# Kernel optimization log

Hardware: AMD Instinct MI355X
Metric: run time of the kernel (lower is better)

Reference implementation:

```python
import jax, jax.numpy as jnp
import numpy as np


def rotary_pos_emb(x):
    # x: [..., seq, dim], dim even. Interleaved (GPT-NeoX-style pairwise) rotary.
    dim, seq = x.shape[-1], x.shape[-2]
    ts = jnp.arange(0, dim, 2, dtype=jnp.float32)
    inv_freqs = 10000.0 ** (-ts / dim)
    grid = jnp.arange(seq, dtype=jnp.float32)[:, None] * inv_freqs[None, :]  # [s, dim//2]
    sin = jnp.repeat(jnp.sin(grid), 2, axis=-1).astype(x.dtype)  # [s, dim]
    cos = jnp.repeat(jnp.cos(grid), 2, axis=-1).astype(x.dtype)  # [s, dim]
    x1, x2 = x[..., ::2], x[..., 1::2]
    xs = jnp.stack([-x2, x1], axis=-1).reshape(x.shape)  # interleave (-x2, x1)
    return x * cos + xs * sin


def setup_inputs() -> dict:
    key = jax.random.key(0)
    kx, kq, kk, kv, ko = jax.random.split(key, 5)
    B, S, D = 2, 2048, 1024
    scale = 1.0 / np.sqrt(D)
    x = jax.random.normal(kx, (B, S, D), dtype=jnp.float32)
    mask = jnp.tril(jnp.ones((S, S), dtype=bool))  # causal
    Wq = jax.random.normal(kq, (D, D), dtype=jnp.float32) * scale
    Wk = jax.random.normal(kk, (D, D), dtype=jnp.float32) * scale
    Wv = jax.random.normal(kv, (D, D), dtype=jnp.float32) * scale
    Wo = jax.random.normal(ko, (D, D), dtype=jnp.float32) * scale
    return {"x": x, "mask": mask, "Wq": Wq, "Wk": Wk, "Wv": Wv, "Wo": Wo}


def reference(x, mask, Wq, Wk, Wv, Wo):
    H = 16
    POS_PORTION = 0.5
    B, S, D = x.shape
    K = D // H
    p = int(K * POS_PORTION)

    q = (x @ Wq) / (K ** 0.5)
    q = q.reshape(B, S, H, K).transpose(0, 2, 1, 3)  # b h l k
    q = jnp.concatenate([rotary_pos_emb(q[..., :p]), q[..., p:]], axis=-1)

    k = (x @ Wk).reshape(B, S, H, K).transpose(0, 2, 1, 3)
    k = jnp.concatenate([rotary_pos_emb(k[..., :p]), k[..., p:]], axis=-1)

    v = (x @ Wv).reshape(B, S, H, K).transpose(0, 2, 1, 3)

    logits = jnp.einsum('bhik,bhjk->bhij', q, k)
    # full-precision masked softmax
    l32 = logits.astype(jnp.float32)
    l32 = jnp.where(mask, l32, -1e30)
    a = jax.nn.softmax(l32, axis=-1).astype(logits.dtype)

    y = jnp.einsum('bhij,bhjv->bhiv', a, v)
    y = y.transpose(0, 2, 1, 3).reshape(B, S, D)  # b l (h v)
    return y @ Wo
```

## Files before the change

### kernel.cpp

```cpp
#include <hip/hip_runtime.h>
#include <cstdint>
#include <cstddef>

typedef __bf16 bf16;
typedef __bf16 bf16x8 __attribute__((ext_vector_type(8)));
typedef float  f32x4  __attribute__((ext_vector_type(4)));

#define B_  2
#define S_  2048
#define D_  1024
#define H_  16
#define KH  64

__device__ __forceinline__ void gload_lds16(const bf16* gp, bf16* lds_base) {
    __builtin_amdgcn_global_load_lds(
        (const __attribute__((address_space(1))) unsigned int*)gp,
        (__attribute__((address_space(3))) unsigned int*)lds_base,
        16, 0, 0);
}

__global__ __launch_bounds__(256) void prep(
    const float* __restrict__ x, bf16* __restrict__ xb,
    const float* __restrict__ Wq, const float* __restrict__ Wk,
    const float* __restrict__ Wv, const float* __restrict__ Wo,
    bf16* __restrict__ WqkvT, bf16* __restrict__ WoT)
{
    __shared__ bf16 tl[64][72];
    int z = blockIdx.x;
    if (z < 4096) {
        const int i = (z * 256 + threadIdx.x) * 4;
        const float4 v = *(const float4*)(x + i);
        union { int2 w; bf16 e[4]; } u;
        u.e[0] = (bf16)v.x; u.e[1] = (bf16)v.y;
        u.e[2] = (bf16)v.z; u.e[3] = (bf16)v.w;
        *(int2*)(xb + i) = u.w;
        return;
    }
    z -= 4096;
    const int zx = z & 15, zy = (z >> 4) & 15, zw = z >> 8;
    const float* src = (zw == 0) ? Wq : (zw == 1) ? Wk : (zw == 2) ? Wv : Wo;
    bf16* dst = (zw < 3) ? (WqkvT + (size_t)zw * D_ * D_) : WoT;
    const int r0 = zy * 64;
    const int c0 = zx * 64;
    const int t  = threadIdx.x;
    {
        const int r = t >> 2, cs = (t & 3) * 16;
        const float4* p = (const float4*)(src + (size_t)(r0 + r) * D_ + c0 + cs);
        float4 a0 = p[0], a1 = p[1], a2 = p[2], a3 = p[3];
        tl[cs +  0][r] = (bf16)a0.x; tl[cs +  1][r] = (bf16)a0.y;
        tl[cs +  2][r] = (bf16)a0.z; tl[cs +  3][r] = (bf16)a0.w;
        tl[cs +  4][r] = (bf16)a1.x; tl[cs +  5][r] = (bf16)a1.y;
        tl[cs +  6][r] = (bf16)a1.z; tl[cs +  7][r] = (bf16)a1.w;
        tl[cs +  8][r] = (bf16)a2.x; tl[cs +  9][r] = (bf16)a2.y;
        tl[cs + 10][r] = (bf16)a2.z; tl[cs + 11][r] = (bf16)a2.w;
        tl[cs + 12][r] = (bf16)a3.x; tl[cs + 13][r] = (bf16)a3.y;
        tl[cs + 14][r] = (bf16)a3.z; tl[cs + 15][r] = (bf16)a3.w;
    }
    __syncthreads();
    {
        const int c = t >> 2, rs = (t & 3) * 16;
        union { int4 v[2]; bf16 e[16]; } u;
#pragma unroll
        for (int i = 0; i < 16; ++i) u.e[i] = tl[c][rs + i];
        int4* p = (int4*)(dst + (size_t)(c0 + c) * D_ + r0 + rs);
        p[0] = u.v[0]; p[1] = u.v[1];
    }
}

template <int EPI, int BN>
__global__ __launch_bounds__(256, 2) void gemm_bt(
    const bf16* __restrict__ A, const bf16* __restrict__ BT,
    float* __restrict__ C, int N, int Kd,
    bf16* __restrict__ qp, bf16* __restrict__ kp, bf16* __restrict__ vp)
{
    constexpr int NJF = BN / 32;
    __shared__ bf16 As[128 * 64];
    __shared__ bf16 Bs[BN * 64];
    const int tid  = threadIdx.x;
    const int lane = tid & 63;
    const int wave = tid >> 6;
    const int l15  = lane & 15;
    const int quad = lane >> 4;
    const int m0 = blockIdx.y * 128;
    const int n0 = blockIdx.x * BN;
    const int wm = (wave >> 1) * 64;
    const int wn = (wave & 1) * (BN / 2);

    f32x4 acc[4][NJF];
#pragma unroll
    for (int i = 0; i < 4; ++i)
#pragma unroll
        for (int j = 0; j < NJF; ++j) acc[i][j] = f32x4{0.f, 0.f, 0.f, 0.f};

    for (int k0 = 0; k0 < Kd; k0 += 64) {
        __syncthreads();
#pragma unroll
        for (int c = 0; c < 4; ++c) {
            const int base  = wave * 4096 + c * 1024;
            const int flatb = base + lane * 16;
            const int row   = flatb >> 7;
            const int col   = (flatb & 127) >> 1;
            gload_lds16(A + (size_t)(m0 + row) * Kd + k0 + col, As + (base >> 1));
        }
#pragma unroll
        for (int c = 0; c < NJF; ++c) {
            const int base  = wave * (BN * 32) + c * 1024;
            const int flatb = base + lane * 16;
            const int row   = flatb >> 7;
            const int col   = (flatb & 127) >> 1;
            gload_lds16(BT + (size_t)(n0 + row) * Kd + k0 + col, Bs + (base >> 1));
        }
        __syncthreads();
#pragma unroll
        for (int kk = 0; kk < 64; kk += 32) {
            bf16x8 af[4], bfv[NJF];
#pragma unroll
            for (int i = 0; i < 4; ++i)
                af[i] = *(const bf16x8*)&As[(wm + i * 16 + l15) * 64 + kk + quad * 8];
#pragma unroll
            for (int j = 0; j < NJF; ++j)
                bfv[j] = *(const bf16x8*)&Bs[(wn + j * 16 + l15) * 64 + kk + quad * 8];
#pragma unroll
            for (int i = 0; i < 4; ++i)
#pragma unroll
                for (int j = 0; j < NJF; ++j)
                    acc[i][j] = __builtin_amdgcn_mfma_f32_16x16x32_bf16(
                        af[i], bfv[j], acc[i][j], 0, 0, 0);
        }
    }

#pragma unroll
    for (int i = 0; i < 4; ++i)
#pragma unroll
        for (int j = 0; j < NJF; ++j) {
            const int Rb = m0 + wm + i * 16 + quad * 4;
            const int Cc = n0 + wn + j * 16 + l15;
            if (EPI == 0) {
#pragma unroll
                for (int r = 0; r < 4; ++r)
                    C[(size_t)(Rb + r) * N + Cc] = acc[i][j][r];
            } else {
                const int sec = Cc >> 10, cc = Cc & 1023;
                const int h = cc >> 6, kd = cc & 63;
#pragma unroll
                for (int r = 0; r < 4; ++r) {
                    const int row = Rb + r;
                    const int b = row >> 11, s = row & (S_ - 1);
                    float v = acc[i][j][r];
                    if (sec == 0) {
                        qp[((size_t)(b * H_ + h) * S_ + s) * KH + kd] =
                            (bf16)(v * 0.1803368801111204f);
                    } else if (sec == 1) {
                        if ((kd >> 4) < 2) {
                            const float partner = __shfl_xor(v, 1);
                            const float inv = __builtin_exp2f(
                                -(float)(kd >> 1) * (13.28771237954945f / 16.f));
                            const float ang = (float)s * inv;
                            float sn, cn;
                            __sincosf(ang, &sn, &cn);
                            v = (l15 & 1) ? fmaf(partner, sn, v * cn)
                                          : fmaf(-partner, sn, v * cn);
                        }
                        kp[((size_t)(b * H_ + h) * S_ + s) * KH + kd] = (bf16)v;
                    } else {
                        vp[((size_t)(b * H_ + h) * KH + kd) * S_ + s] = (bf16)v;
                    }
                }
            }
        }
}

__global__ __launch_bounds__(128, 2) void attn(
    const bf16* __restrict__ q, const bf16* __restrict__ k,
    const bf16* __restrict__ vt, bf16* __restrict__ y)
{
    __shared__ bf16 Ks[2][64 * 64];
    __shared__ bf16 VTs[2][64 * 64];
    __shared__ bf16 Ps[2][2][16][64];

    const int z  = blockIdx.x;
    const int v_ = z & 7;
    const int u_ = (z >> 3) & 31;
    const int w_ = z >> 8;
    const int bh = u_;
    const int qt = (w_ == 0) ? v_ : (w_ == 1) ? (15 - v_)
                 : (w_ == 2) ? (16 + v_) : (31 - v_);
    const int b  = bh >> 4, h = bh & 15;
    const int t    = threadIdx.x;
    const int lane = t & 63, wave = t >> 6;
    const int l15  = lane & 15, quad = lane >> 4;
    const int wrow = qt * 64 + wave * 32;

    const bf16* kbh = k  + (size_t)bh * S_ * KH;
    const bf16* vbh = vt + (size_t)bh * KH * S_;

    const int srow = lane >> 3;
    const int sg   = (lane & 7) ^ srow;

    auto stage = [&](int jt, int bb) {
        const int j0 = jt * 64;
#pragma unroll
        for (int i = 0; i < 4; ++i) {
            const int c = wave * 4 + i;
            gload_lds16(kbh + (size_t)(j0 + c * 8 + srow) * KH + sg * 8,
                        &Ks[bb][c * 8 * 64]);
            gload_lds16(vbh + (size_t)(c * 8 + srow) * S_ + j0 + sg * 8,
                        &VTs[bb][c * 8 * 64]);
        }
    };

    bf16x8 qf[2][2];
#pragma unroll
    for (int mi = 0; mi < 2; ++mi) {
        const bf16* qp = q + ((size_t)bh * S_ + wrow + mi * 16 + l15) * KH + quad * 8;
        qf[mi][0] = *(const bf16x8*)qp;
        qf[mi][1] = *(const bf16x8*)(qp + 32);
        const float s = (float)(wrow + mi * 16 + l15);
#pragma unroll
        for (int tt = 0; tt < 4; ++tt) {
            const int i = quad * 4 + tt;
            const float inv = exp2f(-(float)i * (13.28771237954945f / 16.f));
            const float ang = s * inv;
            const float sn = sinf(ang), cn = cosf(ang);
            const float x0 = (float)qf[mi][0][2 * tt], x1 = (float)qf[mi][0][2 * tt + 1];
            qf[mi][0][2 * tt]     = (bf16)(x0 * cn - x1 * sn);
            qf[mi][0][2 * tt + 1] = (bf16)(x1 * cn + x0 * sn);
        }
    }

    bf16x8 ones;
#pragma unroll
    for (int i = 0; i < 8; ++i) ones[i] = (bf16)1.0f;

    f32x4 accO[2][4], lacc[2];
#pragma unroll
    for (int mi = 0; mi < 2; ++mi) {
#pragma unroll
        for (int j = 0; j < 4; ++j) accO[mi][j] = f32x4{0.f, 0.f, 0.f, 0.f};
        lacc[mi] = f32x4{0.f, 0.f, 0.f, 0.f};
    }

    const int nj = qt + 1;
    stage(0, 0);
    for (int jt = 0; jt < nj; ++jt) {
        const int bb = jt & 1;
        __syncthreads();
        if (jt + 1 < nj) stage(jt + 1, bb ^ 1);

        f32x4 accS[2][4];
#pragma unroll
        for (int mi = 0; mi < 2; ++mi)
#pragma unroll
            for (int nb = 0; nb < 4; ++nb) accS[mi][nb] = f32x4{0.f, 0.f, 0.f, 0.f};
#pragma unroll
        for (int c = 0; c < 2; ++c) {
            bf16x8 kf[4];
#pragma unroll
            for (int nb = 0; nb < 4; ++nb)
                kf[nb] = *(const bf16x8*)
                    &Ks[bb][(nb * 16 + l15) * 64 + (((c * 4 + quad) ^ (l15 & 7)) * 8)];
#pragma unroll
            for (int mi = 0; mi < 2; ++mi)
#pragma unroll
                for (int nb = 0; nb < 4; ++nb)
                    accS[mi][nb] = __builtin_amdgcn_mfma_f32_16x16x32_bf16(
                        qf[mi][c], kf[nb], accS[mi][nb], 0, 0, 0);
        }

        if (jt == nj - 1) {
            const int j0 = jt * 64;
#pragma unroll
            for (int mi = 0; mi < 2; ++mi)
#pragma unroll
                for (int nb = 0; nb < 4; ++nb)
#pragma unroll
                    for (int r = 0; r < 4; ++r) {
                        const int qi = wrow + mi * 16 + quad * 4 + r;
                        const int ki = j0 + nb * 16 + l15;
                        if (ki > qi) accS[mi][nb][r] = -1e30f;
                    }
        }

#pragma unroll
        for (int mi = 0; mi < 2; ++mi)
#pragma unroll
            for (int nb = 0; nb < 4; ++nb)
#pragma unroll
                for (int r = 0; r < 4; ++r) {
                    const float p = __builtin_amdgcn_exp2f(accS[mi][nb][r]);
                    const int row = quad * 4 + r;
                    Ps[wave][mi][row][(((nb * 2 + (l15 >> 3)) ^ (row & 7)) * 8) + (l15 & 7)]
                        = (bf16)p;
                }

#pragma unroll
        for (int c = 0; c < 2; ++c) {
            bf16x8 vf[4];
#pragma unroll
            for (int vb = 0; vb < 4; ++vb)
                vf[vb] = *(const bf16x8*)
                    &VTs[bb][(vb * 16 + l15) * 64 + (((c * 4 + quad) ^ (l15 & 7)) * 8)];
            bf16x8 pf[2];
#pragma unroll
            for (int mi = 0; mi < 2; ++mi)
                pf[mi] = *(const bf16x8*)
                    &Ps[wave][mi][l15][((c * 4 + quad) ^ (l15 & 7)) * 8];
#pragma unroll
            for (int mi = 0; mi < 2; ++mi) {
#pragma unroll
                for (int vb = 0; vb < 4; ++vb)
                    accO[mi][vb] = __builtin_amdgcn_mfma_f32_16x16x32_bf16(
                        pf[mi], vf[vb], accO[mi][vb], 0, 0, 0);
                lacc[mi] = __builtin_amdgcn_mfma_f32_16x16x32_bf16(
                    pf[mi], ones, lacc[mi], 0, 0, 0);
            }
        }
    }

#pragma unroll
    for (int mi = 0; mi < 2; ++mi) {
        float rinv[4];
#pragma unroll
        for (int r = 0; r < 4; ++r) rinv[r] = 1.0f / lacc[mi][r];
#pragma unroll
        for (int vb = 0; vb < 4; ++vb)
#pragma unroll
            for (int r = 0; r < 4; ++r) {
                const int row = wrow + mi * 16 + quad * 4 + r;
                const int col = h * KH + vb * 16 + l15;
                y[((size_t)b * S_ + row) * D_ + col] = (bf16)(accO[mi][vb][r] * rinv[r]);
            }
    }
}

extern "C" void kernel_launch(void* const* d_in, const int* in_sizes, int n_in,
                              void* d_out, int out_size, void* d_ws, size_t ws_size,
                              hipStream_t stream)
{
    (void)in_sizes; (void)n_in; (void)out_size; (void)ws_size;
    const float* x  = (const float*)d_in[0];
    const float* Wq = (const float*)d_in[2];
    const float* Wk = (const float*)d_in[3];
    const float* Wv = (const float*)d_in[4];
    const float* Wo = (const float*)d_in[5];
    float* out = (float*)d_out;

    char* ws = (char*)d_ws;
    bf16* WqkvT = (bf16*)(ws + 0);
    bf16* WoT   = (bf16*)(ws + 6291456);
    bf16* xb    = (bf16*)(ws + 8388608);
    bf16* qw    = (bf16*)(ws + 16777216);
    bf16* kw    = (bf16*)(ws + 25165824);
    bf16* vtw   = (bf16*)(ws + 33554432);
    bf16* yw    = (bf16*)(ws + 41943040);

    hipLaunchKernelGGL(prep, dim3(5120), dim3(256), 0, stream,
                       x, xb, Wq, Wk, Wv, Wo, WqkvT, WoT);
    hipLaunchKernelGGL((gemm_bt<1, 128>), dim3(24, 32), dim3(256), 0, stream,
                       xb, WqkvT, (float*)nullptr, 3072, 1024, qw, kw, vtw);
    hipLaunchKernelGGL(attn, dim3(1024), dim3(128), 0, stream, qw, kw, vtw, yw);
    hipLaunchKernelGGL((gemm_bt<0, 64>), dim3(16, 32), dim3(256), 0, stream,
                       yw, WoT, out, 1024, 1024,
                       (bf16*)nullptr, (bf16*)nullptr, (bf16*)nullptr);
}
```

Before: 203.3 us.

## Use 128-row query tiles with 4 waves and transposed MFMA for packed P stores

The attention kernel now processes 128 query rows per block with 256 threads (4 waves) instead of 64 rows with 2 waves. Each staged K/V tile is therefore shared by twice as many query rows, and each thread issues half as many staging loads. The S and O MFMAs swap operands so each lane holds 4 consecutive keys or output columns. This allows packed 8-byte stores of P into LDS and of y to global memory, and reduces the row-sum to a single value per lane. The trade-off is half as many blocks (512), coarser causal load balancing, and masking on up to two diagonal tiles per wave.

Result: no change. 204.3 us (+0.5%).

```diff
diff --git a/kernel.cpp b/kernel.cpp
--- a/kernel.cpp
+++ b/kernel.cpp
@@ -170,26 +170,25 @@
         }
 }
 
-__global__ __launch_bounds__(128, 2) void attn(
+__global__ __launch_bounds__(256, 2) void attn(
     const bf16* __restrict__ q, const bf16* __restrict__ k,
     const bf16* __restrict__ vt, bf16* __restrict__ y)
 {
     __shared__ bf16 Ks[2][64 * 64];
     __shared__ bf16 VTs[2][64 * 64];
-    __shared__ bf16 Ps[2][2][16][64];
+    __shared__ bf16 Ps[4][2][16][64];
 
     const int z  = blockIdx.x;
     const int v_ = z & 7;
     const int u_ = (z >> 3) & 31;
     const int w_ = z >> 8;
     const int bh = u_;
-    const int qt = (w_ == 0) ? v_ : (w_ == 1) ? (15 - v_)
-                 : (w_ == 2) ? (16 + v_) : (31 - v_);
+    const int qt = w_ ? (15 - v_) : v_;
     const int b  = bh >> 4, h = bh & 15;
     const int t    = threadIdx.x;
     const int lane = t & 63, wave = t >> 6;
     const int l15  = lane & 15, quad = lane >> 4;
-    const int wrow = qt * 64 + wave * 32;
+    const int wrow = qt * 128 + wave * 32;
 
     const bf16* kbh = k  + (size_t)bh * S_ * KH;
     const bf16* vbh = vt + (size_t)bh * KH * S_;
@@ -200,8 +199,8 @@
     auto stage = [&](int jt, int bb) {
         const int j0 = jt * 64;
 #pragma unroll
-        for (int i = 0; i < 4; ++i) {
-            const int c = wave * 4 + i;
+        for (int i = 0; i < 2; ++i) {
+            const int c = wave * 2 + i;
             gload_lds16(kbh + (size_t)(j0 + c * 8 + srow) * KH + sg * 8,
                         &Ks[bb][c * 8 * 64]);
             gload_lds16(vbh + (size_t)(c * 8 + srow) * S_ + j0 + sg * 8,
@@ -240,18 +239,21 @@
         lacc[mi] = f32x4{0.f, 0.f, 0.f, 0.f};
     }
 
-    const int nj = qt + 1;
+    const int psw = (l15 & 7) << 1;
+
+    const int nj = 2 * qt + 2;
     stage(0, 0);
     for (int jt = 0; jt < nj; ++jt) {
         const int bb = jt & 1;
+        const int j0 = jt * 64;
         __syncthreads();
         if (jt + 1 < nj) stage(jt + 1, bb ^ 1);
 
-        f32x4 accS[2][4];
+        f32x4 accST[2][4];
 #pragma unroll
         for (int mi = 0; mi < 2; ++mi)
 #pragma unroll
-            for (int nb = 0; nb < 4; ++nb) accS[mi][nb] = f32x4{0.f, 0.f, 0.f, 0.f};
+            for (int nb = 0; nb < 4; ++nb) accST[mi][nb] = f32x4{0.f, 0.f, 0.f, 0.f};
 #pragma unroll
         for (int c = 0; c < 2; ++c) {
             bf16x8 kf[4];
@@ -263,35 +265,34 @@
             for (int mi = 0; mi < 2; ++mi)
 #pragma unroll
                 for (int nb = 0; nb < 4; ++nb)
-                    accS[mi][nb] = __builtin_amdgcn_mfma_f32_16x16x32_bf16(
-                        qf[mi][c], kf[nb], accS[mi][nb], 0, 0, 0);
-        }
-
-        if (jt == nj - 1) {
-            const int j0 = jt * 64;
+                    accST[mi][nb] = __builtin_amdgcn_mfma_f32_16x16x32_bf16(
+                        kf[nb], qf[mi][c], accST[mi][nb], 0, 0, 0);
+        }
+
+        if (j0 + 63 > wrow) {
 #pragma unroll
             for (int mi = 0; mi < 2; ++mi)
 #pragma unroll
                 for (int nb = 0; nb < 4; ++nb)
 #pragma unroll
                     for (int r = 0; r < 4; ++r) {
-                        const int qi = wrow + mi * 16 + quad * 4 + r;
-                        const int ki = j0 + nb * 16 + l15;
-                        if (ki > qi) accS[mi][nb][r] = -1e30f;
+                        const int ki = j0 + nb * 16 + quad * 4 + r;
+                        const int qi = wrow + mi * 16 + l15;
+                        if (ki > qi) accST[mi][nb][r] = -1e30f;
                     }
         }
 
 #pragma unroll
         for (int mi = 0; mi < 2; ++mi)
 #pragma unroll
-            for (int nb = 0; nb < 4; ++nb)
-#pragma unroll
-                for (int r = 0; r < 4; ++r) {
-                    const float p = __builtin_amdgcn_exp2f(accS[mi][nb][r]);
-                    const int row = quad * 4 + r;
-                    Ps[wave][mi][row][(((nb * 2 + (l15 >> 3)) ^ (row & 7)) * 8) + (l15 & 7)]
-                        = (bf16)p;
-                }
+            for (int nb = 0; nb < 4; ++nb) {
+                union { int2 w; bf16 e[4]; } pk;
+#pragma unroll
+                for (int r = 0; r < 4; ++r)
+                    pk.e[r] = (bf16)__builtin_amdgcn_exp2f(accST[mi][nb][r]);
+                const int gsw = (nb * 4 + quad) ^ psw;
+                *(int2*)&Ps[wave][mi][l15][gsw * 4] = pk.w;
+            }
 
 #pragma unroll
         for (int c = 0; c < 2; ++c) {
@@ -302,34 +303,34 @@
                     &VTs[bb][(vb * 16 + l15) * 64 + (((c * 4 + quad) ^ (l15 & 7)) * 8)];
             bf16x8 pf[2];
 #pragma unroll
-            for (int mi = 0; mi < 2; ++mi)
-                pf[mi] = *(const bf16x8*)
-                    &Ps[wave][mi][l15][((c * 4 + quad) ^ (l15 & 7)) * 8];
+            for (int mi = 0; mi < 2; ++mi) {
+                const int gr = ((c * 8 + quad * 2) ^ psw);
+                pf[mi] = *(const bf16x8*)&Ps[wave][mi][l15][gr * 4];
+            }
 #pragma unroll
             for (int mi = 0; mi < 2; ++mi) {
 #pragma unroll
                 for (int vb = 0; vb < 4; ++vb)
                     accO[mi][vb] = __builtin_amdgcn_mfma_f32_16x16x32_bf16(
-                        pf[mi], vf[vb], accO[mi][vb], 0, 0, 0);
+                        vf[vb], pf[mi], accO[mi][vb], 0, 0, 0);
                 lacc[mi] = __builtin_amdgcn_mfma_f32_16x16x32_bf16(
-                    pf[mi], ones, lacc[mi], 0, 0, 0);
+                    ones, pf[mi], lacc[mi], 0, 0, 0);
             }
         }
     }
 
 #pragma unroll
     for (int mi = 0; mi < 2; ++mi) {
-        float rinv[4];
-#pragma unroll
-        for (int r = 0; r < 4; ++r) rinv[r] = 1.0f / lacc[mi][r];
-#pragma unroll
-        for (int vb = 0; vb < 4; ++vb)
-#pragma unroll
-            for (int r = 0; r < 4; ++r) {
-                const int row = wrow + mi * 16 + quad * 4 + r;
-                const int col = h * KH + vb * 16 + l15;
-                y[((size_t)b * S_ + row) * D_ + col] = (bf16)(accO[mi][vb][r] * rinv[r]);
-            }
+        const float rinv = 1.0f / lacc[mi][0];
+        const int row = wrow + mi * 16 + l15;
+#pragma unroll
+        for (int vb = 0; vb < 4; ++vb) {
+            union { int2 w; bf16 e[4]; } pk;
+#pragma unroll
+            for (int r = 0; r < 4; ++r)
+                pk.e[r] = (bf16)(accO[mi][vb][r] * rinv);
+            *(int2*)&y[((size_t)b * S_ + row) * D_ + h * KH + vb * 16 + quad * 4] = pk.w;
+        }
     }
 }
 
@@ -358,7 +359,7 @@
                        x, xb, Wq, Wk, Wv, Wo, WqkvT, WoT);
     hipLaunchKernelGGL((gemm_bt<1, 128>), dim3(24, 32), dim3(256), 0, stream,
                        xb, WqkvT, (float*)nullptr, 3072, 1024, qw, kw, vtw);
-    hipLaunchKernelGGL(attn, dim3(1024), dim3(128), 0, stream, qw, kw, vtw, yw);
+    hipLaunchKernelGGL(attn, dim3(512), dim3(256), 0, stream, qw, kw, vtw, yw);
     hipLaunchKernelGGL((gemm_bt<0, 64>), dim3(16, 32), dim3(256), 0, stream,
                        yw, WoT, out, 1024, 1024,
                        (bf16*)nullptr, (bf16*)nullptr, (bf16*)nullptr);
```
